# Performance work log

Hardware: AMD Instinct MI355X
Metric: run time of the kernel (lower is better)

The kernel has to match this reference:

```python
import jax, jax.numpy as jnp
import numpy as np

N_NODES = 50000
N_EDGES = 1600000
HIDDEN = 512
LN_EPS = 1e-5


def setup_inputs() -> dict:
    key = jax.random.key(0)
    k1, k2, k3, k4 = jax.random.split(key, 4)
    label_emb = jax.random.normal(k1, (N_NODES, HIDDEN), dtype=jnp.float32)
    edge_index = jax.random.randint(k2, (2, N_EDGES), 0, N_NODES, dtype=jnp.int64)
    W = jax.random.normal(k3, (HIDDEN, HIDDEN), dtype=jnp.float32) / np.sqrt(HIDDEN)
    b = jnp.zeros((HIDDEN,), dtype=jnp.float32)
    gamma = jnp.ones((HIDDEN,), dtype=jnp.float32)
    beta = jnp.zeros((HIDDEN,), dtype=jnp.float32)
    return {"label_emb": label_emb, "edge_index": edge_index, "W": W, "b": b,
            "gamma": gamma, "beta": beta}


def _gcn_conv(x, src, dst, W, b, n_nodes):
    loops = jnp.arange(n_nodes, dtype=src.dtype)
    src_all = jnp.concatenate([src, loops])  # [E+N]
    dst_all = jnp.concatenate([dst, loops])
    ones = jnp.ones_like(dst_all, dtype=x.dtype)
    deg = jax.ops.segment_sum(ones, dst_all, num_segments=n_nodes)  # [N]
    dinv = jnp.where(deg > 0, jax.lax.rsqrt(deg), 0.0)
    norm = dinv[src_all] * dinv[dst_all]  # [E+N]
    h = x @ W  # [N, H] dense transform first (fewer FLOPs than per-edge)
    msgs = h[src_all] * norm[:, None]  # gather + per-edge scale
    out = jax.ops.segment_sum(msgs, dst_all, num_segments=n_nodes)  # scatter-add
    return out + b


def reference(label_emb, edge_index, W, b, gamma, beta):
    residual = label_emb
    src, dst = edge_index[0], edge_index[1]
    h = _gcn_conv(label_emb, src, dst, W, b, N_NODES)
    # dropout is identity at inference (training=False)
    h = residual + h
    mean = jnp.mean(h, axis=-1, keepdims=True)
    var = jnp.var(h, axis=-1, keepdims=True)
    h = (h - mean) * jax.lax.rsqrt(var + LN_EPS) * gamma + beta
    return h
```

## Files before the change

### kernel.cpp

```cpp
#include <hip/hip_runtime.h>
#include <hip/hip_bf16.h>

#define HID 512
#define CAP 128
#define BINCAP 384

typedef unsigned int uint32;
using bf16x8 = __attribute__((ext_vector_type(8))) short;
using f32x4  = __attribute__((ext_vector_type(4))) float;
using f32x2  = __attribute__((ext_vector_type(2))) float;
using u32x2  = __attribute__((ext_vector_type(2))) unsigned int;
using u32x4  = __attribute__((ext_vector_type(4))) unsigned int;
using u16x8  = __attribute__((ext_vector_type(8))) unsigned short;

__device__ __forceinline__ unsigned short f2bf(float f) {
    uint32 u = __float_as_uint(f);
    uint32 r = (u + 0x7FFFu + ((u >> 16) & 1u)) >> 16;
    return (unsigned short)r;
}

__device__ __forceinline__ void gl_lds16(const void* g, void* l) {
    __builtin_amdgcn_global_load_lds(
        (const __attribute__((address_space(1))) void*)g,
        (__attribute__((address_space(3))) void*)l,
        16, 0, 0);
}

__device__ __forceinline__ bf16x8 pack_bf16x8(f32x4 lo, f32x4 hi) {
    union { bf16x8 v; unsigned short u[8]; } r;
    #pragma unroll
    for (int z = 0; z < 4; ++z) {
        union { __hip_bfloat16 h; unsigned short u; } a, b;
        a.h = __float2bfloat16(lo[z]);
        b.h = __float2bfloat16(hi[z]);
        r.u[z] = a.u; r.u[z + 4] = b.u;
    }
    return r.v;
}

__global__ __launch_bounds__(256) void prep_bin(const int* __restrict__ src,
                                                const int* __restrict__ dst,
                                                int* __restrict__ bincnt,
                                                uint32* __restrict__ bins, int e,
                                                const float* __restrict__ W,
                                                unsigned short* __restrict__ Wt,
                                                int nbb) {
    const int bid = blockIdx.x;
    if (bid < nbb) {
        for (int i = bid * 256 + (int)threadIdx.x; i < e; i += nbb * 256) {
            int d = dst[i], s = src[i];
            int b = d >> 3;
            int p = atomicAdd(&bincnt[b], 1);
            bins[(size_t)b * BINCAP + p] = ((uint32)(d & 7) << 16) | (uint32)s;
        }
    } else {
        int idx = (bid - nbb) * 256 + threadIdx.x;
        if (idx < HID * HID) {
            int k = idx >> 9, n = idx & (HID - 1);
            Wt[n * HID + k] = f2bf(W[k * HID + n]);
        }
    }
}

#define NWGX 4
__global__ __launch_bounds__(256) void csr_gemm(const uint32* __restrict__ bins,
                                                const int* __restrict__ bincnt,
                                                unsigned short* __restrict__ csrf,
                                                int* __restrict__ fill,
                                                float* __restrict__ dinvf,
                                                const float* __restrict__ Xf,
                                                const unsigned short* __restrict__ Wt,
                                                unsigned char* __restrict__ hs8,
                                                int nslices, int nwg, int nreal) {
    __shared__ alignas(16) unsigned char smem[49152];

    if ((int)blockIdx.x < nslices) {
        unsigned short* lcs = (unsigned short*)smem;
        int* lcnt = (int*)(smem + 128 * CAP * 2);
        const int b = blockIdx.x;
        for (int j = threadIdx.x; j < 128; j += 256) lcnt[j] = 0;
        __syncthreads();
        #pragma unroll
        for (int sb = 0; sb < 16; ++sb) {
            const int gb = b * 16 + sb;
            const int m = bincnt[gb];
            const uint32* be = bins + (size_t)gb * BINCAP;
            for (int i = threadIdx.x; i < m; i += 256) {
                uint32 ev = be[i];
                int ln = sb * 8 + (int)(ev >> 16);
                int p = atomicAdd(&lcnt[ln], 1);
                lcs[ln * CAP + p] = (unsigned short)(ev & 0xFFFFu);
            }
        }
        __syncthreads();
        u32x4* gout = (u32x4*)(csrf + (size_t)b * 128 * CAP);
        const u32x4* lin = (const u32x4*)lcs;
        for (int j = threadIdx.x; j < 128 * CAP / 8; j += 256) gout[j] = lin[j];
        if (threadIdx.x < 128) {
            int c = lcnt[threadIdx.x];
            fill[b * 128 + threadIdx.x] = c;
            dinvf[b * 128 + threadIdx.x] = rsqrtf((float)c + 1.0f);
        }
        return;
    }

    float* Aldsf = (float*)smem;
    unsigned short* Blds = (unsigned short*)(smem + 32768);
    const int bx = (int)blockIdx.x - nslices;
    const int cpx = nwg >> 3;
    const int swz = (bx & 7) * cpx + (bx >> 3);
    const int row_base = (swz >> 2) * 128;
    const int col_base = (swz & 3) * 128;

    const int t = threadIdx.x;
    const int lane = t & 63, wid = t >> 6;
    const int wm = wid >> 1, wn = wid & 1;

    const int arow4 = lane >> 4;
    const int ach   = (lane & 15) >> 1;
    const int ahalf = lane & 1;
    const int srow = lane >> 3;
    const int gch  = ((lane & 7) ^ srow) * 8;
    const unsigned short* gB = Wt + (size_t)(col_base + wid * 8 + srow) * HID + gch;
    unsigned short* lB = &Blds[wid * 512];

    f32x4 acc[4][4];
    #pragma unroll
    for (int m = 0; m < 4; ++m)
        #pragma unroll
        for (int n = 0; n < 4; ++n)
            acc[m][n] = (f32x4){0.f, 0.f, 0.f, 0.f};

    const int rr = lane & 15;
    const int kg8 = lane >> 4;

    for (int k0 = 0; k0 < HID; k0 += 64) {
        #pragma unroll
        for (int rd = 0; rd < 8; ++rd) {
            int r = wid * 32 + rd * 4 + arow4;
            int grow = row_base + r;
            if (grow >= nreal) grow = nreal - 1;
            int sw = ((ach ^ (r & 7)) << 3) + ahalf * 4;
            gl_lds16(Xf + (size_t)grow * HID + k0 + sw,
                     Aldsf + (size_t)(wid * 32 + rd * 4) * 64);
        }
        #pragma unroll
        for (int rd = 0; rd < 4; ++rd)
            gl_lds16(gB + (size_t)rd * 32 * HID + k0, lB + rd * 2048);
        __syncthreads();

        bf16x8 afr[4][2], bfr[4][2];
        #pragma unroll
        for (int m = 0; m < 4; ++m) {
            int row = wm * 64 + m * 16 + rr;
            #pragma unroll
            for (int ks = 0; ks < 2; ++ks) {
                int off = (((ks * 4 + kg8) ^ (row & 7)) << 3);
                const float* ap = &Aldsf[(size_t)(row << 6) + off];
                f32x4 lo = *(const f32x4*)ap;
                f32x4 hi = *(const f32x4*)(ap + 4);
                afr[m][ks] = pack_bf16x8(lo, hi);
            }
        }
        #pragma unroll
        for (int n = 0; n < 4; ++n) {
            int row = wn * 64 + n * 16 + rr;
            #pragma unroll
            for (int ks = 0; ks < 2; ++ks)
                bfr[n][ks] = *(const bf16x8*)&Blds[row * 64 + (((ks * 4 + kg8) ^ (row & 7)) * 8)];
        }
        #pragma unroll
        for (int ks = 0; ks < 2; ++ks)
            #pragma unroll
            for (int m = 0; m < 4; ++m)
                #pragma unroll
                for (int n = 0; n < 4; ++n)
                    acc[m][n] = __builtin_amdgcn_mfma_f32_16x16x32_bf16(afr[m][ks], bfr[n][ks], acc[m][n], 0, 0, 0);
        __syncthreads();
    }

    const int rgrp = (lane >> 4) * 4;
    const int cc = lane & 15;
    #pragma unroll
    for (int m = 0; m < 4; ++m) {
        #pragma unroll
        for (int r = 0; r < 4; ++r) {
            int grow = row_base + wm * 64 + m * 16 + rgrp + r;
            #pragma unroll
            for (int n = 0; n < 4; ++n) {
                int gcol = col_base + wn * 64 + n * 16 + cc;
                float v = acc[m][n][r];
                unsigned int p = __builtin_amdgcn_cvt_pk_fp8_f32(v, v, 0u, false);
                hs8[(size_t)grow * HID + gcol] = (unsigned char)p;
            }
        }
    }
}

__device__ __forceinline__ void dec8s(u32x2 v, float g, float* acc) {
    f32x2 a = __builtin_amdgcn_cvt_pk_f32_fp8(v[0], false);
    f32x2 b = __builtin_amdgcn_cvt_pk_f32_fp8(v[0], true);
    f32x2 c = __builtin_amdgcn_cvt_pk_f32_fp8(v[1], false);
    f32x2 d = __builtin_amdgcn_cvt_pk_f32_fp8(v[1], true);
    acc[0] += g * a[0]; acc[1] += g * a[1]; acc[2] += g * b[0]; acc[3] += g * b[1];
    acc[4] += g * c[0]; acc[5] += g * c[1]; acc[6] += g * d[0]; acc[7] += g * d[1];
}

__global__ __launch_bounds__(256) void agg_ln(const unsigned char* __restrict__ hs8,
                                              const float* __restrict__ resid,
                                              const float* __restrict__ bvec,
                                              const float* __restrict__ gamma,
                                              const float* __restrict__ beta,
                                              const int* __restrict__ fill,
                                              const float* __restrict__ dinvf,
                                              const unsigned short* __restrict__ csrf,
                                              float* __restrict__ out, int nn) {
    const int wave = threadIdx.x >> 6;
    const int lane = threadIdx.x & 63;
    const int n = blockIdx.x * 4 + wave;
    if (n >= nn) return;
    const int c0 = lane * 8;

    const float gn = dinvf[n];
    float acc[8];
    #pragma unroll
    for (int j = 0; j < 8; ++j) acc[j] = 0.f;
    dec8s(*(const u32x2*)(hs8 + (size_t)n * HID + c0), gn, acc);

    const int m = fill[n];
    const unsigned short* idx = csrf + (size_t)n * CAP;
    int i = 0;
    for (; i + 8 <= m; i += 8) {
        u16x8 iv = *(const u16x8*)(idx + i);
        float g0 = dinvf[iv[0]], g1 = dinvf[iv[1]], g2 = dinvf[iv[2]], g3 = dinvf[iv[3]];
        float g4 = dinvf[iv[4]], g5 = dinvf[iv[5]], g6 = dinvf[iv[6]], g7 = dinvf[iv[7]];
        u32x2 v0 = *(const u32x2*)(hs8 + (size_t)iv[0] * HID + c0);
        u32x2 v1 = *(const u32x2*)(hs8 + (size_t)iv[1] * HID + c0);
        u32x2 v2 = *(const u32x2*)(hs8 + (size_t)iv[2] * HID + c0);
        u32x2 v3 = *(const u32x2*)(hs8 + (size_t)iv[3] * HID + c0);
        u32x2 v4 = *(const u32x2*)(hs8 + (size_t)iv[4] * HID + c0);
        u32x2 v5 = *(const u32x2*)(hs8 + (size_t)iv[5] * HID + c0);
        u32x2 v6 = *(const u32x2*)(hs8 + (size_t)iv[6] * HID + c0);
        u32x2 v7 = *(const u32x2*)(hs8 + (size_t)iv[7] * HID + c0);
        dec8s(v0, g0, acc); dec8s(v1, g1, acc); dec8s(v2, g2, acc); dec8s(v3, g3, acc);
        dec8s(v4, g4, acc); dec8s(v5, g5, acc); dec8s(v6, g6, acc); dec8s(v7, g7, acc);
    }
    for (; i < m; ++i) {
        int s = idx[i];
        dec8s(*(const u32x2*)(hs8 + (size_t)s * HID + c0), dinvf[s], acc);
    }

    f32x4 r0 = __builtin_nontemporal_load((const f32x4*)(resid + (size_t)n * HID + c0));
    f32x4 r1 = __builtin_nontemporal_load((const f32x4*)(resid + (size_t)n * HID + c0 + 4));
    float val[8];
    #pragma unroll
    for (int j = 0; j < 4; ++j) {
        val[j]     = r0[j] + gn * acc[j]     + bvec[c0 + j];
        val[j + 4] = r1[j] + gn * acc[j + 4] + bvec[c0 + j + 4];
    }

    float s = 0.f, q = 0.f;
    #pragma unroll
    for (int j = 0; j < 8; ++j) { s += val[j]; q += val[j] * val[j]; }
    #pragma unroll
    for (int off = 32; off > 0; off >>= 1) {
        s += __shfl_xor(s, off, 64);
        q += __shfl_xor(q, off, 64);
    }
    const float mean = s * (1.f / 512.f);
    const float var = q * (1.f / 512.f) - mean * mean;
    const float rstd = rsqrtf(var + 1e-5f);

    f32x4 o0, o1;
    #pragma unroll
    for (int j = 0; j < 4; ++j) {
        o0[j] = (val[j]     - mean) * rstd * gamma[c0 + j]     + beta[c0 + j];
        o1[j] = (val[j + 4] - mean) * rstd * gamma[c0 + j + 4] + beta[c0 + j + 4];
    }
    __builtin_nontemporal_store(o0, (f32x4*)(out + (size_t)n * HID + c0));
    __builtin_nontemporal_store(o1, (f32x4*)(out + (size_t)n * HID + c0 + 4));
}

extern "C" void kernel_launch(void* const* d_in, const int* in_sizes, int n_in,
                              void* d_out, int out_size, void* d_ws, size_t ws_size,
                              hipStream_t stream) {
    const float* X     = (const float*)d_in[0];
    const int*   edges = (const int*)d_in[1];
    const float* W     = (const float*)d_in[2];
    const float* b     = (const float*)d_in[3];
    const float* gamma = (const float*)d_in[4];
    const float* beta  = (const float*)d_in[5];
    float* out = (float*)d_out;

    const int E = in_sizes[1] / 2;
    const int N = in_sizes[0] / HID;
    const int M_pad = ((N + 255) / 256) * 256;
    const int nslices = M_pad / 128;
    const int nbins = M_pad / 8;
    const int* src = edges;
    const int* dst = edges + E;

    char* w = (char*)d_ws;
    auto alloc = [&](size_t bytes) { char* p = w; w += (bytes + 255) & ~(size_t)255; return p; };
    int*    fill   = (int*)alloc((size_t)M_pad * 4);
    float*  dinvf  = (float*)alloc((size_t)M_pad * 4);
    int*    bincnt = (int*)alloc((size_t)nbins * 4);
    uint32* bins   = (uint32*)alloc((size_t)nbins * BINCAP * 4);
    unsigned short* csrf = (unsigned short*)alloc((size_t)M_pad * CAP * 2);
    unsigned short* Wt   = (unsigned short*)alloc((size_t)HID * HID * 2);
    unsigned char*  hs8  = (unsigned char*)alloc((size_t)M_pad * HID);

    hipMemsetAsync(bincnt, 0, (size_t)nbins * 4, stream);

    const int nbb = 2048;
    const int nbw = (HID * HID + 255) / 256;
    prep_bin<<<nbb + nbw, 256, 0, stream>>>(src, dst, bincnt, bins, E, W, Wt, nbb);

    const int nwg = (M_pad / 128) * NWGX;
    csr_gemm<<<nslices + nwg, 256, 0, stream>>>(bins, bincnt, csrf, fill, dinvf,
                                                X, Wt, hs8, nslices, nwg, N);

    agg_ln<<<(N + 3) / 4, 256, 0, stream>>>(hs8, X, b, gamma, beta, fill, dinvf, csrf, out, N);
}
```

Measured before the change: 272.3 us.

## Halve LDS footprint: K-step 32 GEMM tiles and 64-node CSR slices

```diff
diff --git a/kernel.cpp b/kernel.cpp
--- a/kernel.cpp
+++ b/kernel.cpp
@@ -72,17 +72,17 @@
                                                 const unsigned short* __restrict__ Wt,
                                                 unsigned char* __restrict__ hs8,
                                                 int nslices, int nwg, int nreal) {
-    __shared__ alignas(16) unsigned char smem[49152];
+    __shared__ alignas(16) unsigned char smem[24576];
 
     if ((int)blockIdx.x < nslices) {
         unsigned short* lcs = (unsigned short*)smem;
-        int* lcnt = (int*)(smem + 128 * CAP * 2);
+        int* lcnt = (int*)(smem + 64 * CAP * 2);
         const int b = blockIdx.x;
-        for (int j = threadIdx.x; j < 128; j += 256) lcnt[j] = 0;
+        if (threadIdx.x < 64) lcnt[threadIdx.x] = 0;
         __syncthreads();
         #pragma unroll
-        for (int sb = 0; sb < 16; ++sb) {
-            const int gb = b * 16 + sb;
+        for (int sb = 0; sb < 8; ++sb) {
+            const int gb = b * 8 + sb;
             const int m = bincnt[gb];
             const uint32* be = bins + (size_t)gb * BINCAP;
             for (int i = threadIdx.x; i < m; i += 256) {
@@ -93,19 +93,19 @@
             }
         }
         __syncthreads();
-        u32x4* gout = (u32x4*)(csrf + (size_t)b * 128 * CAP);
+        u32x4* gout = (u32x4*)(csrf + (size_t)b * 64 * CAP);
         const u32x4* lin = (const u32x4*)lcs;
-        for (int j = threadIdx.x; j < 128 * CAP / 8; j += 256) gout[j] = lin[j];
-        if (threadIdx.x < 128) {
+        for (int j = threadIdx.x; j < 64 * CAP / 8; j += 256) gout[j] = lin[j];
+        if (threadIdx.x < 64) {
             int c = lcnt[threadIdx.x];
-            fill[b * 128 + threadIdx.x] = c;
-            dinvf[b * 128 + threadIdx.x] = rsqrtf((float)c + 1.0f);
+            fill[b * 64 + threadIdx.x] = c;
+            dinvf[b * 64 + threadIdx.x] = rsqrtf((float)c + 1.0f);
         }
         return;
     }
 
     float* Aldsf = (float*)smem;
-    unsigned short* Blds = (unsigned short*)(smem + 32768);
+    unsigned short* Blds = (unsigned short*)(smem + 16384);
     const int bx = (int)blockIdx.x - nslices;
     const int cpx = nwg >> 3;
     const int swz = (bx & 7) * cpx + (bx >> 3);
@@ -116,13 +116,8 @@
     const int lane = t & 63, wid = t >> 6;
     const int wm = wid >> 1, wn = wid & 1;
 
-    const int arow4 = lane >> 4;
-    const int ach   = (lane & 15) >> 1;
-    const int ahalf = lane & 1;
-    const int srow = lane >> 3;
-    const int gch  = ((lane & 7) ^ srow) * 8;
-    const unsigned short* gB = Wt + (size_t)(col_base + wid * 8 + srow) * HID + gch;
-    unsigned short* lB = &Blds[wid * 512];
+    const int a_sw = (((lane & 7) ^ (lane >> 3)) << 2);
+    const int b_sw = (((lane & 3) ^ ((lane >> 3) & 3)) << 3);
 
     f32x4 acc[4][4];
     #pragma unroll
@@ -134,48 +129,44 @@
     const int rr = lane & 15;
     const int kg8 = lane >> 4;
 
-    for (int k0 = 0; k0 < HID; k0 += 64) {
-        #pragma unroll
-        for (int rd = 0; rd < 8; ++rd) {
-            int r = wid * 32 + rd * 4 + arow4;
+    for (int k0 = 0; k0 < HID; k0 += 32) {
+        #pragma unroll
+        for (int rd = 0; rd < 4; ++rd) {
+            int r = wid * 32 + rd * 8 + (lane >> 3);
             int grow = row_base + r;
             if (grow >= nreal) grow = nreal - 1;
-            int sw = ((ach ^ (r & 7)) << 3) + ahalf * 4;
-            gl_lds16(Xf + (size_t)grow * HID + k0 + sw,
-                     Aldsf + (size_t)(wid * 32 + rd * 4) * 64);
-        }
-        #pragma unroll
-        for (int rd = 0; rd < 4; ++rd)
-            gl_lds16(gB + (size_t)rd * 32 * HID + k0, lB + rd * 2048);
+            gl_lds16(Xf + (size_t)grow * HID + k0 + a_sw,
+                     Aldsf + (size_t)(wid * 32 + rd * 8) * 32);
+        }
+        #pragma unroll
+        for (int rd = 0; rd < 2; ++rd) {
+            int r = wid * 32 + rd * 16 + (lane >> 2);
+            gl_lds16(Wt + (size_t)(col_base + r) * HID + k0 + b_sw,
+                     Blds + (size_t)(wid * 32 + rd * 16) * 32);
+        }
         __syncthreads();
 
-        bf16x8 afr[4][2], bfr[4][2];
+        bf16x8 afr[4], bfr[4];
         #pragma unroll
         for (int m = 0; m < 4; ++m) {
             int row = wm * 64 + m * 16 + rr;
-            #pragma unroll
-            for (int ks = 0; ks < 2; ++ks) {
-                int off = (((ks * 4 + kg8) ^ (row & 7)) << 3);
-                const float* ap = &Aldsf[(size_t)(row << 6) + off];
-                f32x4 lo = *(const f32x4*)ap;
-                f32x4 hi = *(const f32x4*)(ap + 4);
-                afr[m][ks] = pack_bf16x8(lo, hi);
-            }
+            int lo_c = (((kg8 * 2)     ^ (row & 7)) << 2);
+            int hi_c = (((kg8 * 2 + 1) ^ (row & 7)) << 2);
+            f32x4 lo = *(const f32x4*)&Aldsf[(size_t)(row << 5) + lo_c];
+            f32x4 hi = *(const f32x4*)&Aldsf[(size_t)(row << 5) + hi_c];
+            afr[m] = pack_bf16x8(lo, hi);
         }
         #pragma unroll
         for (int n = 0; n < 4; ++n) {
             int row = wn * 64 + n * 16 + rr;
+            int c = ((kg8 ^ ((row >> 1) & 3)) << 3);
+            bfr[n] = *(const bf16x8*)&Blds[(size_t)(row << 5) + c];
+        }
+        #pragma unroll
+        for (int m = 0; m < 4; ++m)
             #pragma unroll
-            for (int ks = 0; ks < 2; ++ks)
-                bfr[n][ks] = *(const bf16x8*)&Blds[row * 64 + (((ks * 4 + kg8) ^ (row & 7)) * 8)];
-        }
-        #pragma unroll
-        for (int ks = 0; ks < 2; ++ks)
-            #pragma unroll
-            for (int m = 0; m < 4; ++m)
-                #pragma unroll
-                for (int n = 0; n < 4; ++n)
-                    acc[m][n] = __builtin_amdgcn_mfma_f32_16x16x32_bf16(afr[m][ks], bfr[n][ks], acc[m][n], 0, 0, 0);
+            for (int n = 0; n < 4; ++n)
+                acc[m][n] = __builtin_amdgcn_mfma_f32_16x16x32_bf16(afr[m], bfr[n], acc[m][n], 0, 0, 0);
         __syncthreads();
     }
 
@@ -295,7 +286,7 @@
     const int E = in_sizes[1] / 2;
     const int N = in_sizes[0] / HID;
     const int M_pad = ((N + 255) / 256) * 256;
-    const int nslices = M_pad / 128;
+    const int nslices = M_pad / 64;
     const int nbins = M_pad / 8;
     const int* src = edges;
     const int* dst = edges + E;
```

New measurement: 288.2 us. 1.06x slower.
